# Kernel tuning notes

Hardware: AMD Instinct MI355X
Metric: run time of the kernel (lower is better)

## Reference

```python
import jax, jax.numpy as jnp
import numpy as np

N_HEAD = 16
NEG = -1e9

def setup_inputs() -> dict:
    key = jax.random.key(0)
    k1, k2, k3 = jax.random.split(key, 3)
    B, S, NX = 8, 1024, 1024
    x = jax.random.normal(k1, (B, S, NX), dtype=jnp.float32)
    w_attn = jax.random.normal(k2, (NX, 3 * NX), dtype=jnp.float32) * 0.02
    b_attn = jnp.zeros((3 * NX,), dtype=jnp.float32)
    w_proj = jax.random.normal(k3, (NX, NX), dtype=jnp.float32) * 0.02
    b_proj = jnp.zeros((NX,), dtype=jnp.float32)
    return {"x": x, "w_attn": w_attn, "b_attn": b_attn, "w_proj": w_proj, "b_proj": b_proj}

def reference(x, w_attn, b_attn, w_proj, b_proj):
    B, S, NX = x.shape
    H = N_HEAD
    D = NX // H
    qkv = x @ w_attn + b_attn                      # [B,S,3*NX]
    q, k, v = jnp.split(qkv, 3, axis=-1)           # each [B,S,NX]
    q = q.reshape(B, S, H, D)
    k = k.reshape(B, S, H, D)
    v = v.reshape(B, S, H, D)
    # scores with scale (scale=True -> divide by sqrt(head_dim))
    w = jnp.einsum('bqhd,bkhd->bhqk', q, k) / jnp.sqrt(jnp.float32(D))
    tril = jnp.tril(jnp.ones((S, S), dtype=w.dtype))  # causal mask buffer
    w = w * tril + NEG * (1.0 - tril)
    w = jax.nn.softmax(w, axis=-1)                 # dropout is identity at eval
    a = jnp.einsum('bhqk,bkhd->bqhd', w, v)        # [B,S,H,D]
    a = a.reshape(B, S, NX)
    a = a @ w_proj + b_proj
    return a
```

## Files before the change

kernel.cpp:

```cpp
#include <hip/hip_runtime.h>
#include <hip/hip_bf16.h>
#include <stdint.h>

typedef __bf16 bf16x8 __attribute__((ext_vector_type(8)));
typedef float  f32x4  __attribute__((ext_vector_type(4)));
typedef float  f32x16 __attribute__((ext_vector_type(16)));

#define BARRIER() asm volatile("s_barrier" ::: "memory")
#define VMCNT(n)  asm volatile("s_waitcnt vmcnt(" #n ")" ::: "memory")
#define LGKM0()   asm volatile("s_waitcnt lgkmcnt(0)" ::: "memory")
#define SCHED0()  __builtin_amdgcn_sched_barrier(0)

__device__ __forceinline__ void gload_lds16(const void* g, void* l) {
  __builtin_amdgcn_global_load_lds(
      (const __attribute__((address_space(1))) unsigned int*)g,
      (__attribute__((address_space(3))) unsigned int*)l, 16, 0, 0);
}

__global__ void k_cast(const float* __restrict__ in, __bf16* __restrict__ out, int n4) {
  int i = blockIdx.x * blockDim.x + threadIdx.x;
  if (i >= n4) return;
  float4 v = reinterpret_cast<const float4*>(in)[i];
  union { __bf16 h[4]; uint64_t u; } c;
  c.h[0] = (__bf16)v.x; c.h[1] = (__bf16)v.y; c.h[2] = (__bf16)v.z; c.h[3] = (__bf16)v.w;
  *reinterpret_cast<uint64_t*>(out + 4l * i) = c.u;
}

__global__ void k_transpose_cast(const float* __restrict__ in, __bf16* __restrict__ out,
                                 int R, int C) {
  __shared__ float t[32][33];
  const int tx = threadIdx.x & 31, ty = threadIdx.x >> 5;
  const int c0 = blockIdx.x * 32, r0 = blockIdx.y * 32;
#pragma unroll
  for (int rr = 0; rr < 4; ++rr)
    t[ty * 4 + rr][tx] = in[(long)(r0 + ty * 4 + rr) * C + c0 + tx];
  __syncthreads();
#pragma unroll
  for (int rr = 0; rr < 4; ++rr)
    out[(long)(c0 + ty * 4 + rr) * R + r0 + tx] = (__bf16)t[tx][ty * 4 + rr];
}

template <int MODE>
__launch_bounds__(256, 2)
__global__ void k_gemm2(const __bf16* __restrict__ A, const __bf16* __restrict__ Bt,
                        const float* __restrict__ bias, int M, int N, int K, int NBX,
                        __bf16* __restrict__ qo, __bf16* __restrict__ ko,
                        __bf16* __restrict__ vo, float* __restrict__ fo) {
  __shared__ __bf16 lds[2][2][8192];
  const int tid = threadIdx.x;
  const int l = tid & 63, w = tid >> 6;
  const int lm = l & 15, lq = l >> 4;
  const int wm = w >> 1, wn = w & 1;
  const int xcd = blockIdx.x & 7, s = blockIdx.x >> 3;
  const int bn = xcd * NBX + s % NBX;
  const int bm = s / NBX;
  const int nt = K >> 6;

  const int rA = tid >> 3;
  const int scol = (((tid & 7) * 16) ^ ((rA & 7) << 4)) >> 1;
  long a_off[4], b_off[4];
#pragma unroll
  for (int li = 0; li < 4; ++li) {
    a_off[li] = (long)(bm * 128 + li * 32 + rA) * K + scol;
    b_off[li] = (long)(bn * 128 + li * 32 + rA) * K + scol;
  }
#define STAGE(buf, t) { \
    gload_lds16(A + a_off[0] + (long)(t) * 64, &lds[buf][0][tid * 8]); \
    gload_lds16(A + a_off[1] + (long)(t) * 64, &lds[buf][0][2048 + tid * 8]); \
    gload_lds16(A + a_off[2] + (long)(t) * 64, &lds[buf][0][4096 + tid * 8]); \
    gload_lds16(A + a_off[3] + (long)(t) * 64, &lds[buf][0][6144 + tid * 8]); \
    gload_lds16(Bt + b_off[0] + (long)(t) * 64, &lds[buf][1][tid * 8]); \
    gload_lds16(Bt + b_off[1] + (long)(t) * 64, &lds[buf][1][2048 + tid * 8]); \
    gload_lds16(Bt + b_off[2] + (long)(t) * 64, &lds[buf][1][4096 + tid * 8]); \
    gload_lds16(Bt + b_off[3] + (long)(t) * 64, &lds[buf][1][6144 + tid * 8]); }

  const int aswz = (lm & 7) << 4;
  const int cofs0 = ((0 * 64 + lq * 16) ^ aswz) >> 1;
  const int cofs1 = ((1 * 64 + lq * 16) ^ aswz) >> 1;
  const int arow = wm * 64 + lm;
  const int brow = wn * 64 + lm;

  f32x4 acc[4][4] = {};

  STAGE(0, 0);

  for (int t = 0; t < nt; ++t) {
    const int cur = t & 1;
    if (t + 1 < nt) { STAGE(cur ^ 1, t + 1); VMCNT(8); }
    else VMCNT(0);
    BARRIER();
    const __bf16* La = lds[cur][0];
    const __bf16* Lbv = lds[cur][1];
    bf16x8 af[4][2], bfr[4][2];
#pragma unroll
    for (int mi = 0; mi < 4; ++mi) {
      af[mi][0] = *(const bf16x8*)&La[(arow + mi * 16) * 64 + cofs0];
      af[mi][1] = *(const bf16x8*)&La[(arow + mi * 16) * 64 + cofs1];
    }
#pragma unroll
    for (int ni = 0; ni < 4; ++ni) {
      bfr[ni][0] = *(const bf16x8*)&Lbv[(brow + ni * 16) * 64 + cofs0];
      bfr[ni][1] = *(const bf16x8*)&Lbv[(brow + ni * 16) * 64 + cofs1];
    }
    LGKM0(); SCHED0();
    __builtin_amdgcn_s_setprio(1);
#pragma unroll
    for (int ks = 0; ks < 2; ++ks)
#pragma unroll
      for (int mi = 0; mi < 4; ++mi)
#pragma unroll
        for (int ni = 0; ni < 4; ++ni)
          acc[mi][ni] = __builtin_amdgcn_mfma_f32_16x16x32_bf16(af[mi][ks], bfr[ni][ks],
                                                                acc[mi][ni], 0, 0, 0);
    __builtin_amdgcn_s_setprio(0);
    SCHED0();
    BARRIER();
  }

  if (MODE == 0) {
#pragma unroll
    for (int ni = 0; ni < 4; ++ni) {
      const int c = bn * 128 + wn * 64 + ni * 16 + lm;
      const float bv = bias[c];
      const int which = c >> 10, cc = c & 1023, hh = cc >> 6, d = cc & 63;
#pragma unroll
      for (int mi = 0; mi < 4; ++mi)
#pragma unroll
        for (int i = 0; i < 4; ++i) {
          const int r = bm * 128 + wm * 64 + mi * 16 + lq * 4 + i;
          const int b = r >> 10, s_ = r & 1023;
          float fv = acc[mi][ni][i] + bv;
          if (which == 0) fv *= 0.125f;
          const __bf16 v = (__bf16)fv;
          const long hb = (long)(b * 16 + hh);
          if (which == 0)      qo[(hb * 1024 + s_) * 64 + d] = v;
          else if (which == 1) ko[(hb * 1024 + s_) * 64 + d] = v;
          else                 vo[(hb * 64 + d) * 1024 + s_] = v;
        }
    }
  } else {
#pragma unroll
    for (int ni = 0; ni < 4; ++ni) {
      const int c = bn * 128 + wn * 64 + ni * 16 + lm;
      const float bv = bias[c];
#pragma unroll
      for (int mi = 0; mi < 4; ++mi)
#pragma unroll
        for (int i = 0; i < 4; ++i) {
          const int r = bm * 128 + wm * 64 + mi * 16 + lq * 4 + i;
          fo[(long)r * N + c] = acc[mi][ni][i] + bv;
        }
    }
  }
#undef STAGE
}

__device__ __forceinline__ void attn_qtile(const __bf16* __restrict__ Q,
                                           const __bf16* __restrict__ Kh,
                                           const __bf16* __restrict__ Vt,
                                           __bf16* __restrict__ ob,
                                           int b, int h, int qbw, int l) {
  const int lm = l & 31, hi = l >> 5;

  bf16x8 qf[4];
#pragma unroll
  for (int ds = 0; ds < 4; ++ds)
    qf[ds] = *(const bf16x8*)(Q + (long)(qbw + lm) * 64 + ds * 16 + hi * 8);

  f32x16 oacc0 = {}, oacc1 = {};
  float m = -__builtin_inff(), s = 0.f;

  const int nt64 = (qbw >> 6) + 1;
  for (int kt = 0; kt < nt64; ++kt) {
    const int k0 = kt * 64;
    f32x16 st0 = {}, st1 = {};
#pragma unroll
    for (int ds = 0; ds < 4; ++ds) {
      bf16x8 kf0 = *(const bf16x8*)(Kh + (long)(k0 + lm) * 64 + ds * 16 + hi * 8);
      bf16x8 kf1 = *(const bf16x8*)(Kh + (long)(k0 + 32 + lm) * 64 + ds * 16 + hi * 8);
      st0 = __builtin_amdgcn_mfma_f32_32x32x16_bf16(kf0, qf[ds], st0, 0, 0, 0);
      st1 = __builtin_amdgcn_mfma_f32_32x32x16_bf16(kf1, qf[ds], st1, 0, 0, 0);
    }
    if (kt == nt64 - 1) {
      const int q = qbw + lm;
#pragma unroll
      for (int r = 0; r < 16; ++r) {
        const int key = k0 + (r & 3) + 8 * (r >> 2) + 4 * hi;
        if (key > q)      st0[r] = -__builtin_inff();
        if (key + 32 > q) st1[r] = -__builtin_inff();
      }
    }
    float tm = fmaxf(st0[0], st1[0]);
#pragma unroll
    for (int r = 1; r < 16; ++r) tm = fmaxf(tm, fmaxf(st0[r], st1[r]));
    tm = fmaxf(tm, __shfl_xor(tm, 32));
    if (!__all(tm <= m + 8.f)) {
      const float mn = fmaxf(m, tm);
      const float fac = __expf(m - mn);
      m = mn;
      s *= fac;
#pragma unroll
      for (int r = 0; r < 16; ++r) {
        const int qr = (r & 3) + 8 * (r >> 2) + 4 * hi;
        const float fr = __int_as_float(
            __builtin_amdgcn_ds_bpermute(qr * 4, __float_as_int(fac)));
        oacc0[r] *= fr; oacc1[r] *= fr;
      }
    }
    float ts = 0.f;
    unsigned int w8a[8], w8b[8];
#pragma unroll
    for (int t = 0; t < 8; ++t) {
      const float pa_ = __expf(st0[2 * t] - m), pb_ = __expf(st0[2 * t + 1] - m);
      ts += pa_ + pb_;
      union { __bf16 hh[2]; unsigned int u; } pk;
      pk.hh[0] = (__bf16)pa_; pk.hh[1] = (__bf16)pb_;
      w8a[t] = pk.u;
    }
#pragma unroll
    for (int t = 0; t < 8; ++t) {
      const float pa_ = __expf(st1[2 * t] - m), pb_ = __expf(st1[2 * t + 1] - m);
      ts += pa_ + pb_;
      union { __bf16 hh[2]; unsigned int u; } pk;
      pk.hh[0] = (__bf16)pa_; pk.hh[1] = (__bf16)pb_;
      w8b[t] = pk.u;
    }
    ts += __shfl_xor(ts, 32);
    s += ts;
    union { unsigned int wd[4]; bf16x8 v; } pa[4];
    {
      const unsigned int e0 = __shfl_xor(hi ? w8a[0] : w8a[2], 32);
      const unsigned int e1 = __shfl_xor(hi ? w8a[1] : w8a[3], 32);
      const unsigned int e2 = __shfl_xor(hi ? w8a[4] : w8a[6], 32);
      const unsigned int e3 = __shfl_xor(hi ? w8a[5] : w8a[7], 32);
      if (hi) {
        pa[0].wd[0] = e0;     pa[0].wd[1] = e1;     pa[0].wd[2] = w8a[2]; pa[0].wd[3] = w8a[3];
        pa[1].wd[0] = e2;     pa[1].wd[1] = e3;     pa[1].wd[2] = w8a[6]; pa[1].wd[3] = w8a[7];
      } else {
        pa[0].wd[0] = w8a[0]; pa[0].wd[1] = w8a[1]; pa[0].wd[2] = e0;     pa[0].wd[3] = e1;
        pa[1].wd[0] = w8a[4]; pa[1].wd[1] = w8a[5]; pa[1].wd[2] = e2;     pa[1].wd[3] = e3;
      }
    }
    {
      const unsigned int e0 = __shfl_xor(hi ? w8b[0] : w8b[2], 32);
      const unsigned int e1 = __shfl_xor(hi ? w8b[1] : w8b[3], 32);
      const unsigned int e2 = __shfl_xor(hi ? w8b[4] : w8b[6], 32);
      const unsigned int e3 = __shfl_xor(hi ? w8b[5] : w8b[7], 32);
      if (hi) {
        pa[2].wd[0] = e0;     pa[2].wd[1] = e1;     pa[2].wd[2] = w8b[2]; pa[2].wd[3] = w8b[3];
        pa[3].wd[0] = e2;     pa[3].wd[1] = e3;     pa[3].wd[2] = w8b[6]; pa[3].wd[3] = w8b[7];
      } else {
        pa[2].wd[0] = w8b[0]; pa[2].wd[1] = w8b[1]; pa[2].wd[2] = e0;     pa[2].wd[3] = e1;
        pa[3].wd[0] = w8b[4]; pa[3].wd[1] = w8b[5]; pa[3].wd[2] = e2;     pa[3].wd[3] = e3;
      }
    }
#pragma unroll
    for (int t = 0; t < 4; ++t) {
      bf16x8 vf0 = *(const bf16x8*)(Vt + (long)lm * 1024 + k0 + t * 16 + hi * 8);
      bf16x8 vf1 = *(const bf16x8*)(Vt + (long)(32 + lm) * 1024 + k0 + t * 16 + hi * 8);
      oacc0 = __builtin_amdgcn_mfma_f32_32x32x16_bf16(pa[t].v, vf0, oacc0, 0, 0, 0);
      oacc1 = __builtin_amdgcn_mfma_f32_32x32x16_bf16(pa[t].v, vf1, oacc1, 0, 0, 0);
    }
  }
  const float invs = 1.f / s;
#pragma unroll
  for (int r = 0; r < 16; ++r) {
    const int qr = (r & 3) + 8 * (r >> 2) + 4 * hi;
    const float inv = __int_as_float(
        __builtin_amdgcn_ds_bpermute(qr * 4, __float_as_int(invs)));
    const long row = (long)(b * 1024 + qbw + qr) * 1024 + h * 64;
    ob[row + lm]      = (__bf16)(oacc0[r] * inv);
    ob[row + 32 + lm] = (__bf16)(oacc1[r] * inv);
  }
}

__global__ __launch_bounds__(256, 2)
void k_attn(const __bf16* __restrict__ qb_, const __bf16* __restrict__ kb,
            const __bf16* __restrict__ vtb, __bf16* __restrict__ ob) {
  const int l = threadIdx.x & 63, w = threadIdx.x >> 6;
  const int bid = blockIdx.x;
  const int xcd = bid & 7, slot = bid >> 3;
  const int bh = xcd + 8 * (slot >> 2);
  const int j = slot & 3;
  const int wi = j * 4 + w;
  const int b = bh >> 4, h = bh & 15;
  const __bf16* Q  = qb_ + (long)bh * 65536;
  const __bf16* Kh = kb  + (long)bh * 65536;
  const __bf16* Vt = vtb + (long)bh * 65536;
  attn_qtile(Q, Kh, Vt, ob, b, h, wi * 32, l);
  attn_qtile(Q, Kh, Vt, ob, b, h, (31 - wi) * 32, l);
}

extern "C" void kernel_launch(void* const* d_in, const int* in_sizes, int n_in,
                              void* d_out, int out_size, void* d_ws, size_t ws_size,
                              hipStream_t stream) {
  const float* x      = (const float*)d_in[0];
  const float* w_attn = (const float*)d_in[1];
  const float* b_attn = (const float*)d_in[2];
  const float* w_proj = (const float*)d_in[3];
  const float* b_proj = (const float*)d_in[4];
  float* out = (float*)d_out;

  char* ws = (char*)d_ws;
  const size_t SZ_XBF = (size_t)8192 * 1024 * 2;
  __bf16* x_bf = (__bf16*)ws;  ws += SZ_XBF;
  __bf16* wat  = (__bf16*)ws;  ws += (size_t)3072 * 1024 * 2;
  __bf16* wpt  = (__bf16*)ws;  ws += (size_t)1024 * 1024 * 2;
  __bf16* qb   = (__bf16*)ws;  ws += SZ_XBF;
  __bf16* kb   = (__bf16*)ws;  ws += SZ_XBF;
  __bf16* vtb  = (__bf16*)ws;  ws += SZ_XBF;
  __bf16* obf  = (__bf16*)ws;  ws += SZ_XBF;

  k_cast<<<8192, 256, 0, stream>>>(x, x_bf, 2097152);
  k_transpose_cast<<<dim3(96, 32), 256, 0, stream>>>(w_attn, wat, 1024, 3072);
  k_transpose_cast<<<dim3(32, 32), 256, 0, stream>>>(w_proj, wpt, 1024, 1024);
  k_gemm2<0><<<1536, 256, 0, stream>>>(x_bf, wat, b_attn, 8192, 3072, 1024, 3,
                                       qb, kb, vtb, nullptr);
  k_attn<<<512, 256, 0, stream>>>(qb, kb, vtb, obf);
  k_gemm2<1><<<512, 256, 0, stream>>>(obf, wpt, b_proj, 8192, 1024, 1024, 1,
                                      nullptr, nullptr, nullptr, out);
}
```

Baseline: 278.8 us.

## Enlarge GEMM tile to 256x128 with K-step 32 and rebuilt swizzle

The bf16 GEMM kernel now computes a 256x128 output tile per block instead of 128x128, with a K step of 32 instead of 64, a single combined LDS buffer and a 4-way XOR swizzle. Each wave holds 8x4 accumulators, which doubles MFMA work per loaded B fragment and halves the number of blocks launched. The aim is more reuse of B data and fewer global loads per flop. In exchange it raises register pressure, gives fewer blocks for the 256 CUs (256 blocks for the projection GEMM), and doubles the number of barriers per unit of K.

Result: slower. 295.6 us (+6.0%).

```diff
diff --git a/kernel.cpp b/kernel.cpp
--- a/kernel.cpp
+++ b/kernel.cpp
@@ -42,11 +42,11 @@
 
 template <int MODE>
 __launch_bounds__(256, 2)
-__global__ void k_gemm2(const __bf16* __restrict__ A, const __bf16* __restrict__ Bt,
+__global__ void k_gemm3(const __bf16* __restrict__ A, const __bf16* __restrict__ Bt,
                         const float* __restrict__ bias, int M, int N, int K, int NBX,
                         __bf16* __restrict__ qo, __bf16* __restrict__ ko,
                         __bf16* __restrict__ vo, float* __restrict__ fo) {
-  __shared__ __bf16 lds[2][2][8192];
+  __shared__ __bf16 lds[2][12288];
   const int tid = threadIdx.x;
   const int l = tid & 63, w = tid >> 6;
   const int lm = l & 15, lq = l >> 4;
@@ -54,64 +54,55 @@
   const int xcd = blockIdx.x & 7, s = blockIdx.x >> 3;
   const int bn = xcd * NBX + s % NBX;
   const int bm = s / NBX;
-  const int nt = K >> 6;
-
-  const int rA = tid >> 3;
-  const int scol = (((tid & 7) * 16) ^ ((rA & 7) << 4)) >> 1;
-  long a_off[4], b_off[4];
-#pragma unroll
-  for (int li = 0; li < 4; ++li) {
-    a_off[li] = (long)(bm * 128 + li * 32 + rA) * K + scol;
-    b_off[li] = (long)(bn * 128 + li * 32 + rA) * K + scol;
-  }
+  const int nt = K >> 5;
+
+  const int rA = tid >> 2;
+  const int scol = (((tid & 3) * 16) ^ ((rA & 3) << 4)) >> 1;
+  long a_off[4], b_off[2];
+#pragma unroll
+  for (int li = 0; li < 4; ++li)
+    a_off[li] = (long)(bm * 256 + li * 64 + rA) * K + scol;
+#pragma unroll
+  for (int li = 0; li < 2; ++li)
+    b_off[li] = (long)(bn * 128 + li * 64 + rA) * K + scol;
+
 #define STAGE(buf, t) { \
-    gload_lds16(A + a_off[0] + (long)(t) * 64, &lds[buf][0][tid * 8]); \
-    gload_lds16(A + a_off[1] + (long)(t) * 64, &lds[buf][0][2048 + tid * 8]); \
-    gload_lds16(A + a_off[2] + (long)(t) * 64, &lds[buf][0][4096 + tid * 8]); \
-    gload_lds16(A + a_off[3] + (long)(t) * 64, &lds[buf][0][6144 + tid * 8]); \
-    gload_lds16(Bt + b_off[0] + (long)(t) * 64, &lds[buf][1][tid * 8]); \
-    gload_lds16(Bt + b_off[1] + (long)(t) * 64, &lds[buf][1][2048 + tid * 8]); \
-    gload_lds16(Bt + b_off[2] + (long)(t) * 64, &lds[buf][1][4096 + tid * 8]); \
-    gload_lds16(Bt + b_off[3] + (long)(t) * 64, &lds[buf][1][6144 + tid * 8]); }
-
-  const int aswz = (lm & 7) << 4;
-  const int cofs0 = ((0 * 64 + lq * 16) ^ aswz) >> 1;
-  const int cofs1 = ((1 * 64 + lq * 16) ^ aswz) >> 1;
-  const int arow = wm * 64 + lm;
+    gload_lds16(A + a_off[0] + (long)(t) * 32, &lds[buf][tid * 8]); \
+    gload_lds16(A + a_off[1] + (long)(t) * 32, &lds[buf][2048 + tid * 8]); \
+    gload_lds16(A + a_off[2] + (long)(t) * 32, &lds[buf][4096 + tid * 8]); \
+    gload_lds16(A + a_off[3] + (long)(t) * 32, &lds[buf][6144 + tid * 8]); \
+    gload_lds16(Bt + b_off[0] + (long)(t) * 32, &lds[buf][8192 + tid * 8]); \
+    gload_lds16(Bt + b_off[1] + (long)(t) * 32, &lds[buf][10240 + tid * 8]); }
+
+  const int cofs = ((lq * 16) ^ ((lm & 3) << 4)) >> 1;
+  const int arow = wm * 128 + lm;
   const int brow = wn * 64 + lm;
 
-  f32x4 acc[4][4] = {};
+  f32x4 acc[8][4] = {};
 
   STAGE(0, 0);
 
   for (int t = 0; t < nt; ++t) {
     const int cur = t & 1;
-    if (t + 1 < nt) { STAGE(cur ^ 1, t + 1); VMCNT(8); }
+    if (t + 1 < nt) { STAGE(cur ^ 1, t + 1); VMCNT(6); }
     else VMCNT(0);
     BARRIER();
-    const __bf16* La = lds[cur][0];
-    const __bf16* Lbv = lds[cur][1];
-    bf16x8 af[4][2], bfr[4][2];
-#pragma unroll
-    for (int mi = 0; mi < 4; ++mi) {
-      af[mi][0] = *(const bf16x8*)&La[(arow + mi * 16) * 64 + cofs0];
-      af[mi][1] = *(const bf16x8*)&La[(arow + mi * 16) * 64 + cofs1];
-    }
-#pragma unroll
-    for (int ni = 0; ni < 4; ++ni) {
-      bfr[ni][0] = *(const bf16x8*)&Lbv[(brow + ni * 16) * 64 + cofs0];
-      bfr[ni][1] = *(const bf16x8*)&Lbv[(brow + ni * 16) * 64 + cofs1];
-    }
+    const __bf16* Lb = lds[cur];
+    bf16x8 af[8], bfr[4];
+#pragma unroll
+    for (int mi = 0; mi < 8; ++mi)
+      af[mi] = *(const bf16x8*)&Lb[(arow + mi * 16) * 32 + cofs];
+#pragma unroll
+    for (int ni = 0; ni < 4; ++ni)
+      bfr[ni] = *(const bf16x8*)&Lb[8192 + (brow + ni * 16) * 32 + cofs];
     LGKM0(); SCHED0();
     __builtin_amdgcn_s_setprio(1);
 #pragma unroll
-    for (int ks = 0; ks < 2; ++ks)
-#pragma unroll
-      for (int mi = 0; mi < 4; ++mi)
-#pragma unroll
-        for (int ni = 0; ni < 4; ++ni)
-          acc[mi][ni] = __builtin_amdgcn_mfma_f32_16x16x32_bf16(af[mi][ks], bfr[ni][ks],
-                                                                acc[mi][ni], 0, 0, 0);
+    for (int mi = 0; mi < 8; ++mi)
+#pragma unroll
+      for (int ni = 0; ni < 4; ++ni)
+        acc[mi][ni] = __builtin_amdgcn_mfma_f32_16x16x32_bf16(af[mi], bfr[ni],
+                                                              acc[mi][ni], 0, 0, 0);
     __builtin_amdgcn_s_setprio(0);
     SCHED0();
     BARRIER();
@@ -124,10 +115,10 @@
       const float bv = bias[c];
       const int which = c >> 10, cc = c & 1023, hh = cc >> 6, d = cc & 63;
 #pragma unroll
-      for (int mi = 0; mi < 4; ++mi)
+      for (int mi = 0; mi < 8; ++mi)
 #pragma unroll
         for (int i = 0; i < 4; ++i) {
-          const int r = bm * 128 + wm * 64 + mi * 16 + lq * 4 + i;
+          const int r = bm * 256 + wm * 128 + mi * 16 + lq * 4 + i;
           const int b = r >> 10, s_ = r & 1023;
           float fv = acc[mi][ni][i] + bv;
           if (which == 0) fv *= 0.125f;
@@ -144,10 +135,10 @@
       const int c = bn * 128 + wn * 64 + ni * 16 + lm;
       const float bv = bias[c];
 #pragma unroll
-      for (int mi = 0; mi < 4; ++mi)
+      for (int mi = 0; mi < 8; ++mi)
 #pragma unroll
         for (int i = 0; i < 4; ++i) {
-          const int r = bm * 128 + wm * 64 + mi * 16 + lq * 4 + i;
+          const int r = bm * 256 + wm * 128 + mi * 16 + lq * 4 + i;
           fo[(long)r * N + c] = acc[mi][ni][i] + bv;
         }
     }
@@ -314,9 +305,9 @@
   k_cast<<<8192, 256, 0, stream>>>(x, x_bf, 2097152);
   k_transpose_cast<<<dim3(96, 32), 256, 0, stream>>>(w_attn, wat, 1024, 3072);
   k_transpose_cast<<<dim3(32, 32), 256, 0, stream>>>(w_proj, wpt, 1024, 1024);
-  k_gemm2<0><<<1536, 256, 0, stream>>>(x_bf, wat, b_attn, 8192, 3072, 1024, 3,
-                                       qb, kb, vtb, nullptr);
+  k_gemm3<0><<<768, 256, 0, stream>>>(x_bf, wat, b_attn, 8192, 3072, 1024, 3,
+                                      qb, kb, vtb, nullptr);
   k_attn<<<512, 256, 0, stream>>>(qb, kb, vtb, obf);
-  k_gemm2<1><<<512, 256, 0, stream>>>(obf, wpt, b_proj, 8192, 1024, 1024, 1,
+  k_gemm3<1><<<256, 256, 0, stream>>>(obf, wpt, b_proj, 8192, 1024, 1024, 1,
                                       nullptr, nullptr, nullptr, out);
 }
```
